# Performance work log

Measured on AMD Instinct MI355X. Metric: run time of the kernel, lower is better.

## Reference

```python
import jax, jax.numpy as jnp
import numpy as np

B, C, W, H, D = 4, 32, 64, 64, 64


def setup_inputs() -> dict:
    key = jax.random.key(0)
    ks = jax.random.split(key, 8)
    x = jax.random.normal(ks[0], (B, C, W, H, D), dtype=jnp.float32)
    # 1x1x1 Conv3d == per-voxel channel mixing: weight (C_out, C_in), bias (C_out,)
    Wq = jax.random.normal(ks[1], (C, C), dtype=jnp.float32) * 0.05
    bq = jax.random.normal(ks[2], (C,), dtype=jnp.float32) * 0.05
    Wk = jax.random.normal(ks[3], (C, C), dtype=jnp.float32) * 0.05
    bk = jax.random.normal(ks[4], (C,), dtype=jnp.float32) * 0.05
    Wv = jax.random.normal(ks[5], (C, C), dtype=jnp.float32) * 0.05
    bv = jax.random.normal(ks[6], (C,), dtype=jnp.float32) * 0.05
    gamma = jnp.float32(0.1)  # torch inits to 0; nonzero so output depends on attention
    return {"x": x, "Wq": Wq, "bq": bq, "Wk": Wk, "bk": bk, "Wv": Wv, "bv": bv, "gamma": gamma}


def reference(x, Wq, bq, Wk, bk, Wv, bv, gamma):
    b, c, w, h, d = x.shape
    N = w * h * d

    def proj(Wt, bt):
        # 1x1x1 conv then torch's .view(b, -1, c): a raw row-major reshape of
        # (b, c, w, h, d) -> (b, N, c) that interleaves channel/spatial (faithful).
        y = jnp.einsum('oc,bcwhd->bowhd', Wt, x) + bt[None, :, None, None, None]
        return y.reshape(b, N, c)

    q = proj(Wq, bq)  # (b, N, c)
    k = proj(Wk, bk)
    v = proj(Wv, bv)
    s = jnp.einsum('bnc,bnd->bcd', q, k)          # q^T k: tiny (b, c, c)
    a = jax.nn.softmax(s, axis=-1)
    scores = jnp.einsum('bnc,bcd->bnd', v, a)     # (b, N, c)
    return x + gamma * scores.reshape(b, c, w, h, d)
```

## Files before the change

### kernel.cpp

```cpp
#include <hip/hip_runtime.h>

typedef __attribute__((ext_vector_type(8))) short bf16x8;
typedef __attribute__((ext_vector_type(4))) float f32x4;

#define MSP   262144
#define BATCH 4
#define TPOS  256
#define NT    8
#define NBLK  (MSP / TPOS / NT)

#define LROW1 258
#define TSZ1  (32 * LROW1)

#define OFF_P  0
#define OFF_CS 4096

#define GLDS16(gsrc, ldst)                                               \
  __builtin_amdgcn_global_load_lds(                                      \
      (const __attribute__((address_space(1))) unsigned int*)(gsrc),     \
      (__attribute__((address_space(3))) unsigned int*)(ldst), 16, 0, 0)

__device__ __forceinline__ unsigned short f2bf(float f) {
  unsigned int u = __float_as_uint(f);
  u += 0x7fffu + ((u >> 16) & 1u);
  return (unsigned short)(u >> 16);
}
__device__ __forceinline__ void split2(float f, short* hi, short* lo) {
  unsigned int u = __float_as_uint(f);
  unsigned int uh = u + (0x7fffu + ((u >> 16) & 1u));
  *hi = (short)(uh >> 16);
  const float r = f - __uint_as_float(uh & 0xffff0000u);
  *lo = (short)(__float_as_uint(r) >> 16);
}

#define MFMA(A, B, C) __builtin_amdgcn_mfma_f32_16x16x32_bf16(A, B, C, 0, 0, 0)


__global__ __launch_bounds__(256) void pass1_kernel(
    const float* __restrict__ x, const float* __restrict__ Wq,
    const float* __restrict__ Wk, float* __restrict__ ws) {
  __shared__ float XT[2 * TSZ1];
  const int tid = threadIdx.x;
  const int w = tid >> 6, l = tid & 63, lm = tid & 15, lb = (tid >> 4) & 3;
  const int b = blockIdx.y;
  const size_t xbase = (size_t)b * 32 * MSP;
  const int tile0 = blockIdx.x * NT;

  const float* rowsrc[8];
#pragma unroll
  for (int rr = 0; rr < 8; ++rr)
    rowsrc[rr] = x + xbase + (size_t)(w * 8 + rr) * MSP + l * 4;

#pragma unroll
  for (int rr = 0; rr < 8; ++rr)
    GLDS16(rowsrc[rr] + tile0 * TPOS, &XT[(w * 8 + rr) * LROW1]);

  {
    float* WqL = XT + TSZ1;
    float* WkL = XT + TSZ1 + 1024;
    for (int k = tid; k < 1024; k += 256) { WqL[k] = Wq[k]; WkL[k] = Wk[k]; }
    __syncthreads();
    float* UL = XT + TSZ1 + 2048;
    for (int k = tid; k < 1024; k += 256) {
      const int aa = k >> 5, bb = k & 31;
      float s = 0.f;
#pragma unroll
      for (int ch = 0; ch < 32; ++ch)
        s = fmaf(WqL[ch * 32 + aa], WkL[ch * 32 + bb], s);
      UL[k] = s;
    }
    __syncthreads();
  }
  bf16x8 uh0, ul0, uh1, ul1;
  {
    const float* UL = XT + TSZ1 + 2048;
#pragma unroll
    for (int r = 0; r < 8; ++r) {
      const int kk = (r < 4) ? lb * 4 + r : 16 + lb * 4 + (r - 4);
      short h, lo;
      split2(UL[lm * 32 + kk], &h, &lo);        uh0[r] = h; ul0[r] = lo;
      split2(UL[(16 + lm) * 32 + kk], &h, &lo); uh1[r] = h; ul1[r] = lo;
    }
  }
  __syncthreads();

  int ldsoff[8];
#pragma unroll
  for (int r = 0; r < 8; ++r) {
    const int ch = (r < 4) ? lb * 4 + r : 16 + lb * 4 + (r - 4);
    ldsoff[r] = ch * LROW1 + lm;
  }

  f32x4 p00 = {0, 0, 0, 0}, p01 = {0, 0, 0, 0}, p10 = {0, 0, 0, 0}, p11 = {0, 0, 0, 0};
  float cs0[8], cs1[8];
#pragma unroll
  for (int r = 0; r < 8; ++r) { cs0[r] = 0.f; cs1[r] = 0.f; }

#pragma unroll 1
  for (int t = 0; t < NT; ++t) {
    const int cur = t & 1;
    if (t + 1 < NT) {
      const int posn = (tile0 + t + 1) * TPOS;
#pragma unroll
      for (int rr = 0; rr < 8; ++rr)
        GLDS16(rowsrc[rr] + posn, &XT[(cur ^ 1) * TSZ1 + (w * 8 + rr) * LROW1]);
    }
    const float* XB = XT + cur * TSZ1;

#pragma unroll
    for (int g2 = 0; g2 < 2; ++g2) {
      const int pl = (w * 2 + g2) * 32;
      float xf0[8], xf1[8];
#pragma unroll
      for (int r = 0; r < 8; ++r) {
        xf0[r] = XB[ldsoff[r] + pl];
        xf1[r] = XB[ldsoff[r] + pl + 16];
      }
      bf16x8 xh0, xl0, xh1, xl1;
#pragma unroll
      for (int r = 0; r < 8; ++r) {
        short h, lo;
        split2(xf0[r], &h, &lo); xh0[r] = h; xl0[r] = lo;
        split2(xf1[r], &h, &lo); xh1[r] = h; xl1[r] = lo;
        cs0[r] += xf0[r];  cs1[r] += xf1[r];
      }

      f32x4 y00 = {0,0,0,0}, y01 = {0,0,0,0}, y10 = {0,0,0,0}, y11 = {0,0,0,0};
      y00 = MFMA(uh0, xh0, y00); y00 = MFMA(uh0, xl0, y00); y00 = MFMA(ul0, xh0, y00);
      y01 = MFMA(uh1, xh0, y01); y01 = MFMA(uh1, xl0, y01); y01 = MFMA(ul1, xh0, y01);
      y10 = MFMA(uh0, xh1, y10); y10 = MFMA(uh0, xl1, y10); y10 = MFMA(ul0, xh1, y10);
      y11 = MFMA(uh1, xh1, y11); y11 = MFMA(uh1, xl1, y11); y11 = MFMA(ul1, xh1, y11);

      bf16x8 yh0, yl0, yh1, yl1;
#pragma unroll
      for (int r = 0; r < 4; ++r) {
        short h, lo;
        split2(y00[r], &h, &lo); yh0[r] = h; yl0[r] = lo;
        split2(y10[r], &h, &lo); yh1[r] = h; yl1[r] = lo;
      }
#pragma unroll
      for (int r = 4; r < 8; ++r) {
        short h, lo;
        split2(y01[r - 4], &h, &lo); yh0[r] = h; yl0[r] = lo;
        split2(y11[r - 4], &h, &lo); yh1[r] = h; yl1[r] = lo;
      }

      p00 = MFMA(xh0, yh0, p00); p00 = MFMA(xh0, yl0, p00); p00 = MFMA(xl0, yh0, p00);
      p01 = MFMA(xh0, yh1, p01); p01 = MFMA(xh0, yl1, p01); p01 = MFMA(xl0, yh1, p01);
      p10 = MFMA(xh1, yh0, p10); p10 = MFMA(xh1, yl0, p10); p10 = MFMA(xl1, yh0, p10);
      p11 = MFMA(xh1, yh1, p11); p11 = MFMA(xh1, yl1, p11); p11 = MFMA(xl1, yh1, p11);
    }
    __syncthreads();
  }

  float* red = XT;
#pragma unroll
  for (int r = 0; r < 4; ++r) {
    red[w * 1024 + (lb * 4 + r) * 32 + lm]           = p00[r];
    red[w * 1024 + (lb * 4 + r) * 32 + 16 + lm]      = p01[r];
    red[w * 1024 + (16 + lb * 4 + r) * 32 + lm]      = p10[r];
    red[w * 1024 + (16 + lb * 4 + r) * 32 + 16 + lm] = p11[r];
  }
  __syncthreads();
  for (int k = tid; k < 1024; k += 256) {
    const float s = red[k] + red[1024 + k] + red[2048 + k] + red[3072 + k];
    atomicAdd(&ws[OFF_P + b * 1024 + k], s);
  }
  __syncthreads();
#pragma unroll
  for (int r = 0; r < 8; ++r) {
    const int ch = (r < 4) ? lb * 4 + r : 16 + lb * 4 + (r - 4);
    red[w * 1024 + ch * 32 + lm]      = cs0[r];
    red[w * 1024 + ch * 32 + 16 + lm] = cs1[r];
  }
  __syncthreads();
  for (int k = tid; k < 1024; k += 256) {
    const float s = red[k] + red[1024 + k] + red[2048 + k] + red[3072 + k];
    atomicAdd(&ws[OFF_CS + b * 1024 + k], s);
  }
}

__global__ __launch_bounds__(256) void pass2_kernel(
    const float* __restrict__ x, const float* __restrict__ Wq,
    const float* __restrict__ bq, const float* __restrict__ Wk,
    const float* __restrict__ bk, const float* __restrict__ Wv,
    const float* __restrict__ bv, const float* __restrict__ gm,
    const float* __restrict__ ws, float* __restrict__ out) {
  __shared__ float XT[2 * 8192];
  __shared__ float Sm[1024];
  __shared__ float u_l[32], v_l[32], su_l[32], sv_l[32], ca_l[32];
  __shared__ float beta_l;

  const int tid = threadIdx.x;
  const int w = tid >> 6, l = tid & 63, lm = tid & 15, lb = (tid >> 4) & 3;
  const int b = blockIdx.y;
  const size_t xbase = (size_t)b * 32 * MSP;
  const int tile0 = blockIdx.x * NT;

#pragma unroll
  for (int rr = 0; rr < 8; ++rr) {
    const int row = w * 8 + rr;
    const int csrc = ((l + rr) & 63) << 2;
    GLDS16(x + xbase + (size_t)row * MSP + tile0 * TPOS + csrc, &XT[row * 256]);
  }

  if (tid < 32) {
    float u = 0.f;
#pragma unroll
    for (int ch = 0; ch < 32; ++ch) u = fmaf(Wq[ch * 32 + tid], bk[ch], u);
    u_l[tid] = u;
  } else if (tid < 64) {
    const int j = tid - 32;
    float v = 0.f;
#pragma unroll
    for (int ch = 0; ch < 32; ++ch) v = fmaf(bq[ch], Wk[ch * 32 + j], v);
    v_l[j] = v;
  } else if (tid == 64) {
    float bt = 0.f;
#pragma unroll
    for (int ch = 0; ch < 32; ++ch) bt = fmaf(bq[ch], bk[ch], bt);
    beta_l = bt;
  }
  __syncthreads();
  if (tid < 32) {
    float s = 0.f;
#pragma unroll
    for (int a = 0; a < 32; ++a)
      s = fmaf(u_l[a], ws[OFF_CS + b * 1024 + a * 32 + tid], s);
    su_l[tid] = s;
  } else if (tid < 64) {
    const int j = tid - 32;
    float s = 0.f;
#pragma unroll
    for (int a = 0; a < 32; ++a)
      s = fmaf(v_l[a], ws[OFF_CS + b * 1024 + a * 32 + j], s);
    sv_l[j] = s;
  }
  __syncthreads();
  {
    const int si = tid >> 3, sj0 = (tid & 7) * 4;
    float s4[4];
#pragma unroll
    for (int c = 0; c < 4; ++c)
      s4[c] = ws[OFF_P + b * 1024 + si * 32 + sj0 + c] + su_l[si] +
              sv_l[sj0 + c] + 8192.0f * beta_l;
    float mx = fmaxf(fmaxf(s4[0], s4[1]), fmaxf(s4[2], s4[3]));
    mx = fmaxf(mx, __shfl_xor(mx, 1, 8));
    mx = fmaxf(mx, __shfl_xor(mx, 2, 8));
    mx = fmaxf(mx, __shfl_xor(mx, 4, 8));
    float e4[4], sum = 0.f;
#pragma unroll
    for (int c = 0; c < 4; ++c) { e4[c] = expf(s4[c] - mx); sum += e4[c]; }
    sum += __shfl_xor(sum, 1, 8);
    sum += __shfl_xor(sum, 2, 8);
    sum += __shfl_xor(sum, 4, 8);
    const float inv = 1.0f / sum;
#pragma unroll
    for (int c = 0; c < 4; ++c) Sm[si * 32 + sj0 + c] = e4[c] * inv;
  }
  __syncthreads();
  if (tid < 32) {
    float c = 0.f;
#pragma unroll
    for (int ii = 0; ii < 32; ++ii) c += Sm[ii * 32 + tid];
    ca_l[tid] = c;
  }
  bf16x8 a0, a1, wv0, wv1;
#pragma unroll
  for (int r = 0; r < 8; ++r) {
    const int kk = (r < 4) ? lb * 4 + r : 16 + lb * 4 + (r - 4);
    a0[r]  = (short)f2bf(Sm[kk * 32 + lm]);
    a1[r]  = (short)f2bf(Sm[kk * 32 + 16 + lm]);
    wv0[r] = (short)f2bf(Wv[lm * 32 + kk]);
    wv1[r] = (short)f2bf(Wv[(16 + lm) * 32 + kk]);
  }
  __syncthreads();

  const float gamma = gm[0];
  const float bv0 = bv[lm], bv1 = bv[16 + lm];
  float i00[4], i01[4], i10[4], i11[4];
#pragma unroll
  for (int r = 0; r < 4; ++r) {
    const float c0 = ca_l[lb * 4 + r];
    const float c1 = ca_l[16 + lb * 4 + r];
    i00[r] = bv0 * c0; i01[r] = bv1 * c0;
    i10[r] = bv0 * c1; i11[r] = bv1 * c1;
  }

  const int c3 = lm & 3, q = lm >> 2;
  int fbase[8], dr[8];
#pragma unroll
  for (int r = 0; r < 8; ++r) {
    const int ch = (r < 4) ? lb * 4 + r : 16 + lb * 4 + (r - 4);
    fbase[r] = ch * 256 + c3;
    dr[r] = q - (ch & 7);
  }
  const int dres = lb - (lm & 7);

#pragma unroll 1
  for (int t = 0; t < NT; ++t) {
    const int cur = t & 1;
    if (t + 1 < NT) {
      const int posn = (tile0 + t + 1) * TPOS;
#pragma unroll
      for (int rr = 0; rr < 8; ++rr) {
        const int row = w * 8 + rr;
        const int csrc = ((l + rr) & 63) << 2;
        GLDS16(x + xbase + (size_t)row * MSP + posn + csrc,
               &XT[(cur ^ 1) * 8192 + row * 256]);
      }
    }
    const float* XB = XT + cur * 8192;
    const int pos0 = (tile0 + t) * TPOS;

#pragma unroll
    for (int g2 = 0; g2 < 2; ++g2) {
      const int pl4 = (w * 2 + g2) * 8;
      bf16x8 xh0, xh1;
#pragma unroll
      for (int r = 0; r < 8; ++r) {
        const int f0 = fbase[r] + (((pl4 + dr[r]) & 63) << 2);
        const int f1 = fbase[r] + (((pl4 + 4 + dr[r]) & 63) << 2);
        xh0[r] = (short)f2bf(XB[f0]);
        xh1[r] = (short)f2bf(XB[f1]);
      }
      f32x4 v00 = {0,0,0,0}, v01 = {0,0,0,0}, v10 = {0,0,0,0}, v11 = {0,0,0,0};
      v00 = MFMA(xh0, wv0, v00); v01 = MFMA(xh0, wv1, v01);
      v10 = MFMA(xh1, wv0, v10); v11 = MFMA(xh1, wv1, v11);

      bf16x8 vb0, vb1;
#pragma unroll
      for (int r = 0; r < 4; ++r) { vb0[r] = (short)f2bf(v00[r]); vb1[r] = (short)f2bf(v01[r]); }
#pragma unroll
      for (int r = 4; r < 8; ++r) { vb0[r] = (short)f2bf(v10[r - 4]); vb1[r] = (short)f2bf(v11[r - 4]); }

      f32x4 t00 = {i00[0], i00[1], i00[2], i00[3]};
      f32x4 t01 = {i01[0], i01[1], i01[2], i01[3]};
      f32x4 t10 = {i10[0], i10[1], i10[2], i10[3]};
      f32x4 t11 = {i11[0], i11[1], i11[2], i11[3]};
      t00 = MFMA(a0, vb0, t00); t01 = MFMA(a0, vb1, t01);
      t10 = MFMA(a1, vb0, t10); t11 = MFMA(a1, vb1, t11);

#define EPI(TT, MT, CT)                                                           \
      {                                                                           \
        const int F = ((CT) * 16 + lm) * 256 +                                    \
                      (((pl4 + (MT) * 4 + dres) & 63) << 2);                      \
        const f32x4 xr = *reinterpret_cast<const f32x4*>(&XB[F]);                 \
        const size_t addr = xbase + (size_t)((CT) * 16 + lm) * MSP +              \
                            (size_t)(pos0 + (pl4 << 2) + (MT) * 16 + lb * 4);     \
        f32x4 o;                                                                  \
        o[0] = fmaf(gamma, TT[0], xr[0]); o[1] = fmaf(gamma, TT[1], xr[1]);       \
        o[2] = fmaf(gamma, TT[2], xr[2]); o[3] = fmaf(gamma, TT[3], xr[3]);       \
        *reinterpret_cast<f32x4*>(out + addr) = o;                                \
      }
      EPI(t00, 0, 0); EPI(t01, 0, 1); EPI(t10, 1, 0); EPI(t11, 1, 1);
#undef EPI
    }
    __syncthreads();
  }
}

extern "C" void kernel_launch(void* const* d_in, const int* in_sizes, int n_in,
                              void* d_out, int out_size, void* d_ws, size_t ws_size,
                              hipStream_t stream) {
  const float* x  = (const float*)d_in[0];
  const float* Wq = (const float*)d_in[1];
  const float* bq = (const float*)d_in[2];
  const float* Wk = (const float*)d_in[3];
  const float* bk = (const float*)d_in[4];
  const float* Wv = (const float*)d_in[5];
  const float* bv = (const float*)d_in[6];
  const float* gm = (const float*)d_in[7];
  float* out = (float*)d_out;
  float* ws  = (float*)d_ws;

  hipMemsetAsync(ws, 0, 8192 * sizeof(float), stream);
  pass1_kernel<<<dim3(NBLK, BATCH), 256, 0, stream>>>(x, Wq, Wk, ws);
  pass2_kernel<<<dim3(NBLK, BATCH), 256, 0, stream>>>(x, Wq, bq, Wk, bk, Wv, bv,
                                                      gm, ws, out);
}
```

Baseline: 83.81 us.

## Give each wave private double-buffered tiles and drop block-wide barriers

Each wave now streams its own contiguous run of positions into a private pair of LDS tiles, instead of the whole block sharing a 256-position tile. This replaces the per-iteration __syncthreads with per-wave s_waitcnt vmcnt counting, so the four waves can proceed independently. The LDS layout changes to a padded per-wave tile, which removes the rotated-column indexing used in pass2. The risk is that the hand-written vmcnt counts are fragile: the pass2 counts must also account for outstanding stores, and a wrong count would read LDS before the async loads land.

```diff
diff --git a/kernel.cpp b/kernel.cpp
--- a/kernel.cpp
+++ b/kernel.cpp
@@ -5,12 +5,11 @@
 
 #define MSP   262144
 #define BATCH 4
-#define TPOS  256
 #define NT    8
-#define NBLK  (MSP / TPOS / NT)
-
-#define LROW1 258
-#define TSZ1  (32 * LROW1)
+#define NBLK  128
+
+#define CSF   264
+#define WTILE (8 * CSF)
 
 #define OFF_P  0
 #define OFF_CS 4096
@@ -39,28 +38,30 @@
 __global__ __launch_bounds__(256) void pass1_kernel(
     const float* __restrict__ x, const float* __restrict__ Wq,
     const float* __restrict__ Wk, float* __restrict__ ws) {
-  __shared__ float XT[2 * TSZ1];
+  __shared__ float XT[8 * WTILE];
+  __shared__ float UW[3072];
   const int tid = threadIdx.x;
   const int w = tid >> 6, l = tid & 63, lm = tid & 15, lb = (tid >> 4) & 3;
   const int b = blockIdx.y;
   const size_t xbase = (size_t)b * 32 * MSP;
-  const int tile0 = blockIdx.x * NT;
-
-  const float* rowsrc[8];
-#pragma unroll
-  for (int rr = 0; rr < 8; ++rr)
-    rowsrc[rr] = x + xbase + (size_t)(w * 8 + rr) * MSP + l * 4;
-
-#pragma unroll
-  for (int rr = 0; rr < 8; ++rr)
-    GLDS16(rowsrc[rr] + tile0 * TPOS, &XT[(w * 8 + rr) * LROW1]);
+  const int wbase = (blockIdx.x * 4 + w) * (NT * 64);
+
+  const int srow = l >> 4;
+  const int scol = (l & 15) * 4;
+  float* wbuf0 = XT + (w * 2 + 0) * WTILE;
+  float* wbuf1 = XT + (w * 2 + 1) * WTILE;
+
+#pragma unroll
+  for (int c = 0; c < 8; ++c)
+    GLDS16(x + xbase + (size_t)(c * 4 + srow) * MSP + wbase + scol,
+           wbuf0 + c * CSF);
 
   {
-    float* WqL = XT + TSZ1;
-    float* WkL = XT + TSZ1 + 1024;
+    float* WqL = UW;
+    float* WkL = UW + 1024;
     for (int k = tid; k < 1024; k += 256) { WqL[k] = Wq[k]; WkL[k] = Wk[k]; }
     __syncthreads();
-    float* UL = XT + TSZ1 + 2048;
+    float* UL = UW + 2048;
     for (int k = tid; k < 1024; k += 256) {
       const int aa = k >> 5, bb = k & 31;
       float s = 0.f;
@@ -73,7 +74,7 @@
   }
   bf16x8 uh0, ul0, uh1, ul1;
   {
-    const float* UL = XT + TSZ1 + 2048;
+    const float* UL = UW + 2048;
 #pragma unroll
     for (int r = 0; r < 8; ++r) {
       const int kk = (r < 4) ? lb * 4 + r : 16 + lb * 4 + (r - 4);
@@ -82,13 +83,12 @@
       split2(UL[(16 + lm) * 32 + kk], &h, &lo); uh1[r] = h; ul1[r] = lo;
     }
   }
-  __syncthreads();
 
   int ldsoff[8];
 #pragma unroll
   for (int r = 0; r < 8; ++r) {
     const int ch = (r < 4) ? lb * 4 + r : 16 + lb * 4 + (r - 4);
-    ldsoff[r] = ch * LROW1 + lm;
+    ldsoff[r] = (ch >> 2) * CSF + (ch & 3) * 64 + lm;
   }
 
   f32x4 p00 = {0, 0, 0, 0}, p01 = {0, 0, 0, 0}, p10 = {0, 0, 0, 0}, p11 = {0, 0, 0, 0};
@@ -98,18 +98,23 @@
 
 #pragma unroll 1
   for (int t = 0; t < NT; ++t) {
-    const int cur = t & 1;
+    const float* XB = (t & 1) ? wbuf1 : wbuf0;
+    float* XN = (t & 1) ? wbuf0 : wbuf1;
     if (t + 1 < NT) {
-      const int posn = (tile0 + t + 1) * TPOS;
-#pragma unroll
-      for (int rr = 0; rr < 8; ++rr)
-        GLDS16(rowsrc[rr] + posn, &XT[(cur ^ 1) * TSZ1 + (w * 8 + rr) * LROW1]);
-    }
-    const float* XB = XT + cur * TSZ1;
+      const int posn = wbase + (t + 1) * 64;
+#pragma unroll
+      for (int c = 0; c < 8; ++c)
+        GLDS16(x + xbase + (size_t)(c * 4 + srow) * MSP + posn + scol,
+               XN + c * CSF);
+      asm volatile("s_waitcnt vmcnt(8)" ::: "memory");
+    } else {
+      asm volatile("s_waitcnt vmcnt(0)" ::: "memory");
+    }
+    __builtin_amdgcn_sched_barrier(0);
 
 #pragma unroll
     for (int g2 = 0; g2 < 2; ++g2) {
-      const int pl = (w * 2 + g2) * 32;
+      const int pl = g2 * 32;
       float xf0[8], xf1[8];
 #pragma unroll
       for (int r = 0; r < 8; ++r) {
@@ -150,9 +155,9 @@
       p10 = MFMA(xh1, yh0, p10); p10 = MFMA(xh1, yl0, p10); p10 = MFMA(xl1, yh0, p10);
       p11 = MFMA(xh1, yh1, p11); p11 = MFMA(xh1, yl1, p11); p11 = MFMA(xl1, yh1, p11);
     }
-    __syncthreads();
-  }
-
+  }
+
+  __syncthreads();
   float* red = XT;
 #pragma unroll
   for (int r = 0; r < 4; ++r) {
@@ -186,7 +191,7 @@
     const float* __restrict__ bk, const float* __restrict__ Wv,
     const float* __restrict__ bv, const float* __restrict__ gm,
     const float* __restrict__ ws, float* __restrict__ out) {
-  __shared__ float XT[2 * 8192];
+  __shared__ float XT[8 * WTILE];
   __shared__ float Sm[1024];
   __shared__ float u_l[32], v_l[32], su_l[32], sv_l[32], ca_l[32];
   __shared__ float beta_l;
@@ -195,14 +200,17 @@
   const int w = tid >> 6, l = tid & 63, lm = tid & 15, lb = (tid >> 4) & 3;
   const int b = blockIdx.y;
   const size_t xbase = (size_t)b * 32 * MSP;
-  const int tile0 = blockIdx.x * NT;
-
-#pragma unroll
-  for (int rr = 0; rr < 8; ++rr) {
-    const int row = w * 8 + rr;
-    const int csrc = ((l + rr) & 63) << 2;
-    GLDS16(x + xbase + (size_t)row * MSP + tile0 * TPOS + csrc, &XT[row * 256]);
-  }
+  const int wbase = (blockIdx.x * 4 + w) * (NT * 64);
+
+  const int srow = l >> 4;
+  const int scol = (l & 15) * 4;
+  float* wbuf0 = XT + (w * 2 + 0) * WTILE;
+  float* wbuf1 = XT + (w * 2 + 1) * WTILE;
+
+#pragma unroll
+  for (int c = 0; c < 8; ++c)
+    GLDS16(x + xbase + (size_t)(c * 4 + srow) * MSP + wbase + scol,
+           wbuf0 + c * CSF);
 
   if (tid < 32) {
     float u = 0.f;
@@ -287,42 +295,48 @@
     i10[r] = bv0 * c1; i11[r] = bv1 * c1;
   }
 
-  const int c3 = lm & 3, q = lm >> 2;
-  int fbase[8], dr[8];
+  int ldsoff[8];
 #pragma unroll
   for (int r = 0; r < 8; ++r) {
     const int ch = (r < 4) ? lb * 4 + r : 16 + lb * 4 + (r - 4);
-    fbase[r] = ch * 256 + c3;
-    dr[r] = q - (ch & 7);
-  }
-  const int dres = lb - (lm & 7);
+    ldsoff[r] = (ch >> 2) * CSF + (ch & 3) * 64 + lm;
+  }
+  int resoff[2][2];
+#pragma unroll
+  for (int CT = 0; CT < 2; ++CT)
+#pragma unroll
+    for (int MT = 0; MT < 2; ++MT)
+      resoff[CT][MT] = (CT * 4 + (lm >> 2)) * CSF + (lm & 3) * 64 +
+                       MT * 16 + lb * 4;
 
 #pragma unroll 1
   for (int t = 0; t < NT; ++t) {
-    const int cur = t & 1;
+    const float* XB = (t & 1) ? wbuf1 : wbuf0;
+    float* XN = (t & 1) ? wbuf0 : wbuf1;
     if (t + 1 < NT) {
-      const int posn = (tile0 + t + 1) * TPOS;
-#pragma unroll
-      for (int rr = 0; rr < 8; ++rr) {
-        const int row = w * 8 + rr;
-        const int csrc = ((l + rr) & 63) << 2;
-        GLDS16(x + xbase + (size_t)row * MSP + posn + csrc,
-               &XT[(cur ^ 1) * 8192 + row * 256]);
-      }
-    }
-    const float* XB = XT + cur * 8192;
-    const int pos0 = (tile0 + t) * TPOS;
+      const int posn = wbase + (t + 1) * 64;
+#pragma unroll
+      for (int c = 0; c < 8; ++c)
+        GLDS16(x + xbase + (size_t)(c * 4 + srow) * MSP + posn + scol,
+               XN + c * CSF);
+      if (t == 0)
+        asm volatile("s_waitcnt vmcnt(8)" ::: "memory");
+      else
+        asm volatile("s_waitcnt vmcnt(16)" ::: "memory");
+    } else {
+      asm volatile("s_waitcnt vmcnt(8)" ::: "memory");
+    }
+    __builtin_amdgcn_sched_barrier(0);
+    const int post = wbase + t * 64;
 
 #pragma unroll
     for (int g2 = 0; g2 < 2; ++g2) {
-      const int pl4 = (w * 2 + g2) * 8;
+      const int pl = g2 * 32;
       bf16x8 xh0, xh1;
 #pragma unroll
       for (int r = 0; r < 8; ++r) {
-        const int f0 = fbase[r] + (((pl4 + dr[r]) & 63) << 2);
-        const int f1 = fbase[r] + (((pl4 + 4 + dr[r]) & 63) << 2);
-        xh0[r] = (short)f2bf(XB[f0]);
-        xh1[r] = (short)f2bf(XB[f1]);
+        xh0[r] = (short)f2bf(XB[ldsoff[r] + pl]);
+        xh1[r] = (short)f2bf(XB[ldsoff[r] + pl + 16]);
       }
       f32x4 v00 = {0,0,0,0}, v01 = {0,0,0,0}, v10 = {0,0,0,0}, v11 = {0,0,0,0};
       v00 = MFMA(xh0, wv0, v00); v01 = MFMA(xh0, wv1, v01);
@@ -343,11 +357,9 @@
 
 #define EPI(TT, MT, CT)                                                           \
       {                                                                           \
-        const int F = ((CT) * 16 + lm) * 256 +                                    \
-                      (((pl4 + (MT) * 4 + dres) & 63) << 2);                      \
-        const f32x4 xr = *reinterpret_cast<const f32x4*>(&XB[F]);                 \
+        const f32x4 xr = *reinterpret_cast<const f32x4*>(&XB[resoff[CT][MT] + pl]); \
         const size_t addr = xbase + (size_t)((CT) * 16 + lm) * MSP +              \
-                            (size_t)(pos0 + (pl4 << 2) + (MT) * 16 + lb * 4);     \
+                            (size_t)(post + pl + (MT) * 16 + lb * 4);             \
         f32x4 o;                                                                  \
         o[0] = fmaf(gamma, TT[0], xr[0]); o[1] = fmaf(gamma, TT[1], xr[1]);       \
         o[2] = fmaf(gamma, TT[2], xr[2]); o[3] = fmaf(gamma, TT[3], xr[3]);       \
@@ -356,7 +368,6 @@
       EPI(t00, 0, 0); EPI(t01, 0, 1); EPI(t10, 1, 0); EPI(t11, 1, 1);
 #undef EPI
     }
-    __syncthreads();
   }
 }
 
```

Result: no change. 82.53 us (-1.5%).
